# Optimization experiments

Hardware: AMD Instinct MI355X
Metric: run time of the kernel (lower is better)

## Reference

```python
import jax, jax.numpy as jnp
import numpy as np

N_NODES = 50000
N_EDGES = 800000
MUL = 16            # multiplicity of each irrep (16x0e + 16x1o)
RADIAL_IN = 8       # radial basis size
RADIAL_HID = 64
N_PATHS = 5         # TP paths: s*Y0->s, v.Yv->s, s*Yv->v, v*Y0->v, v x Yv->v
NUM_SPECIES = 4
AVG_NEIGH = 16.0


def setup_inputs() -> dict:
    key = jax.random.key(0)
    ks = jax.random.split(key, 16)
    inp = {
        'node_scalars': jax.random.normal(ks[0], (N_NODES, MUL), jnp.float32),
        'node_vectors': jax.random.normal(ks[1], (N_NODES, MUL * 3), jnp.float32),
        'edge_sh': jax.random.normal(ks[2], (N_EDGES, 4), jnp.float32),
        'radial_emb': jax.random.uniform(ks[3], (N_EDGES, RADIAL_IN), jnp.float32),
        'senders': jax.random.randint(ks[4], (N_EDGES,), 0, N_NODES, jnp.int32),
        'receivers': jax.random.randint(ks[5], (N_EDGES,), 0, N_NODES, jnp.int32),
        'species': jax.random.randint(ks[6], (N_NODES,), 0, NUM_SPECIES, jnp.int32),
        # learned params (fan-in scaled)
        'W_in_s': jax.random.normal(ks[7], (MUL, MUL), jnp.float32) / np.sqrt(MUL),
        'W_in_v': jax.random.normal(ks[8], (MUL, MUL), jnp.float32) / np.sqrt(MUL),
        'mlp_w1': jax.random.normal(ks[9], (RADIAL_IN, RADIAL_HID), jnp.float32) / np.sqrt(RADIAL_IN),
        'mlp_b1': jnp.zeros((RADIAL_HID,), jnp.float32),
        'mlp_w2': jax.random.normal(ks[10], (RADIAL_HID, N_PATHS * MUL), jnp.float32) / np.sqrt(RADIAL_HID),
        'W_out_s': jax.random.normal(ks[11], (2 * MUL, 2 * MUL), jnp.float32) / np.sqrt(2 * MUL),
        'W_out_v': jax.random.normal(ks[12], (3 * MUL, MUL), jnp.float32) / np.sqrt(3 * MUL),
        'sc_s': jax.random.normal(ks[13], (NUM_SPECIES, MUL, 2 * MUL), jnp.float32) / np.sqrt(MUL),
        'sc_v': jax.random.normal(ks[14], (NUM_SPECIES, MUL, MUL), jnp.float32) / np.sqrt(MUL),
    }
    return inp


def reference(node_scalars, node_vectors, edge_sh, radial_emb, senders, receivers,
              species, W_in_s, W_in_v, mlp_w1, mlp_b1, mlp_w2, W_out_s, W_out_v,
              sc_s, sc_v):
    N = node_scalars.shape[0]
    inv_sqrt_deg = 1.0 / np.sqrt(AVG_NEIGH)

    # ---- input per-irrep linear ----
    s = node_scalars @ W_in_s                                  # [N,16]
    v_in = node_vectors.reshape(N, MUL, 3)
    v = jnp.einsum('nuc,uw->nwc', v_in, W_in_v)                # [N,16,3]

    # ---- gather sender features ----
    xs = s[senders]                                            # [E,16]
    xv = v[senders]                                            # [E,16,3]
    Y0 = edge_sh[:, :1]                                        # [E,1] l=0 SH
    Yv = edge_sh[:, 1:4]                                       # [E,3] l=1 SH

    # ---- radial MLP -> per-path tensor-product weights ----
    h = jax.nn.silu(radial_emb @ mlp_w1 + mlp_b1)              # [E,64]
    w = (h @ mlp_w2).reshape(-1, N_PATHS, MUL)                 # [E,5,16]

    # ---- CG tensor product (uvu) messages ----
    m_s1 = w[:, 0] * xs * Y0                                   # 0e x 0e -> 0e
    m_s2 = w[:, 1] * jnp.einsum('euc,ec->eu', xv, Yv)          # 1o x 1o -> 0e (dot)
    m_v1 = w[:, 2, :, None] * xs[:, :, None] * Yv[:, None, :]  # 0e x 1o -> 1o
    m_v2 = w[:, 3, :, None] * xv * Y0[:, :, None]              # 1o x 0e -> 1o
    m_v3 = w[:, 4, :, None] * jnp.cross(xv, Yv[:, None, :])    # 1o x 1o -> 1o (cross)

    # ---- scatter-sum to receivers + neighbour normalization ----
    m_s = jnp.concatenate([m_s1, m_s2], axis=-1)               # [E,32]
    m_v = jnp.concatenate([m_v1, m_v2, m_v3], axis=1)          # [E,48,3]
    a_s = jax.ops.segment_sum(m_s, receivers, num_segments=N) * inv_sqrt_deg
    a_v = jax.ops.segment_sum(m_v, receivers, num_segments=N) * inv_sqrt_deg

    # ---- output per-irrep linear ----
    pre_s = a_s @ W_out_s                                      # [N,32]
    pre_v = jnp.einsum('nuc,uw->nwc', a_v, W_out_v)            # [N,16,3]

    # ---- species-dependent self connection ----
    pre_s = pre_s + jnp.einsum('nu,nuw->nw', node_scalars, sc_s[species])
    pre_v = pre_v + jnp.einsum('nuc,nuw->nwc', v_in, sc_v[species])

    # ---- gate nonlinearity ----
    out_s = jax.nn.silu(pre_s[:, :MUL])                        # scalar outputs
    gates = jax.nn.sigmoid(pre_s[:, MUL:])                     # gate scalars
    out_v = pre_v * gates[:, :, None]

    # ---- resnet ----
    out_s = out_s + node_scalars
    out_v = out_v + v_in

    return jnp.concatenate([out_s, out_v.reshape(N, MUL * 3)], axis=-1)
```

## Files before the change

kernel.cpp:

```cpp
#include <hip/hip_runtime.h>
#include <hip/hip_bf16.h>

typedef unsigned short u16;
typedef unsigned int   u32;
typedef _Float16 h2 __attribute__((ext_vector_type(2)));
typedef short s8v __attribute__((ext_vector_type(8)));
typedef float f4v __attribute__((ext_vector_type(4)));
typedef u16 u16x4 __attribute__((ext_vector_type(4)));

#define N_NODES 50000
#define N_EDGES 800000
#define NCH   4
#define RPC   12500
#define CHMAX 204800

#define RPB   250
#define NBINS 200
#define EPB   4096
#define NBB   ((N_EDGES+EPB-1)/EPB)

#define WB_W1H  0
#define WB_B1   256
#define WB_W2F  320
#define WB_WINS 2880
#define WB_WINV 3136
#define WB_WOS  3392
#define WB_WOV  4416
#define WB_SCS  5184
#define WB_SCV  7232
#define WB_FLAG 8256
#define OFF_SV16 8260
#define IDX_BCNT 1608260
#define IDX_BOF2 1608516
#define IDX_BCUR 1608772
#define IDX_OFFS 1658260
#define IDX_BUCK 1758262
#define OFF_WP   2558264
#define ACC_OFF  15665472
#define IDX_EEID 17865472
#define OFF_ER16 18665472

__device__ __forceinline__ float bf2f(u16 v){
  union { u32 u; float f; } x; x.u = ((u32)v) << 16; return x.f;
}
__device__ __forceinline__ u16 f2bf(float f){
  u32 u = __float_as_uint(f);
  u32 lsb = (u >> 16) & 1u;
  u32 r = u + 0x7fffu + lsb;
  return (u16)(r >> 16);
}
__device__ __forceinline__ float ldx(const void* p, long long i, int isf){
  return isf ? ((const float*)p)[i] : bf2f(((const u16*)p)[i]);
}
__device__ __forceinline__ u32 pkh2(float a, float b){
  union { u32 u; h2 v; } x; x.v.x = (_Float16)a; x.v.y = (_Float16)b; return x.u;
}
__device__ __forceinline__ float dot2(h2 a, u32 w, float c){
  union { u32 u; h2 v; } x; x.u = w;
#if __has_builtin(__builtin_amdgcn_fdot2)
  return __builtin_amdgcn_fdot2(a, x.v, c, false);
#else
  return c + (float)a.x*(float)x.v.x + (float)a.y*(float)x.v.y;
#endif
}
__device__ __forceinline__ float sigmoidf_(float x){ return 1.f/(1.f + __expf(-x)); }

__global__ void detect_dtype(const u32* __restrict__ remb_raw, int* __restrict__ flag){
  int t = threadIdx.x;
  u32 w = remb_raw[t];
  u32 lo = w & 0xffffu, hi = w >> 16;
  int okl = ((lo & 0x8000u) == 0) && (((lo >> 7) & 0xffu) <= 126u);
  int okh = ((hi & 0x8000u) == 0) && (((hi >> 7) & 0xffu) <= 126u);
  unsigned long long bad = __ballot(!(okl && okh));
  if (t == 0) *flag = (bad != 0ull) ? 1 : 0;
}

__global__ void prep_weights(const void* __restrict__ w1, const void* __restrict__ b1g,
                             const void* __restrict__ w2, const void* __restrict__ wins,
                             const void* __restrict__ winv, const void* __restrict__ wos,
                             const void* __restrict__ wov, const void* __restrict__ scs,
                             const void* __restrict__ scv, float* __restrict__ wbuf,
                             const int* __restrict__ flag){
  int t = threadIdx.x;
  int isf = *flag;
  u32* w1h  = (u32*)(wbuf + WB_W1H);
  u16* w2f  = (u16*)(wbuf + WB_W2F);
  for (int idx=t; idx<256;  idx+=256){
    int j = idx>>2, ip = idx&3;
    w1h[idx] = pkh2(ldx(w1, (2*ip)*64+j, isf), ldx(w1, (2*ip+1)*64+j, isf));
  }
  for (int idx=t; idx<64;   idx+=256){ wbuf[WB_B1+idx]  = ldx(b1g, idx, isf); }
  for (int idx=t; idx<5120; idx+=256){
    int tt = idx >> 10;
    int rem = idx & 1023;
    int kh = rem >> 9;
    int rem2 = rem & 511;
    int ln = rem2 >> 3, j = rem2 & 7;
    int k = kh*32 + (ln>>4)*8 + j;
    int o = tt*16 + (ln&15);
    w2f[idx] = f2bf(ldx(w2, (long long)k*80 + o, isf));
  }
  for (int idx=t; idx<256;  idx+=256){ wbuf[WB_WINS+idx] = ldx(wins, idx, isf); }
  for (int idx=t; idx<256;  idx+=256){ wbuf[WB_WINV+idx] = ldx(winv, idx, isf); }
  for (int idx=t; idx<1024; idx+=256){ wbuf[WB_WOS+idx]  = ldx(wos, idx, isf); }
  for (int idx=t; idx<768;  idx+=256){ wbuf[WB_WOV+idx]  = ldx(wov, idx, isf); }
  for (int idx=t; idx<2048; idx+=256){ wbuf[WB_SCS+idx]  = ldx(scs, idx, isf); }
  for (int idx=t; idx<1024; idx+=256){ wbuf[WB_SCV+idx]  = ldx(scv, idx, isf); }
}

__global__ void __launch_bounds__(64) node_pre(
    const void* __restrict__ ns_g, const void* __restrict__ nv_g,
    const float* __restrict__ wbuf, u16* __restrict__ sv16,
    const int* __restrict__ flag){
  int n = blockIdx.x*64 + threadIdx.x;
  if (n >= N_NODES) return;
  int isf = *flag;
  float a[16], b[48];
  if (isf){
    const f4v* pa = (const f4v*)ns_g + (size_t)n*4;
    #pragma unroll
    for (int k=0;k<4;k++){
      f4v v = pa[k];
      a[k*4]=v[0]; a[k*4+1]=v[1]; a[k*4+2]=v[2]; a[k*4+3]=v[3];
    }
    const f4v* pb = (const f4v*)nv_g + (size_t)n*12;
    #pragma unroll
    for (int k=0;k<12;k++){
      f4v v = pb[k];
      b[k*4]=v[0]; b[k*4+1]=v[1]; b[k*4+2]=v[2]; b[k*4+3]=v[3];
    }
  } else {
    const s8v* pa = (const s8v*)ns_g + (size_t)n*2;
    #pragma unroll
    for (int k=0;k<2;k++){
      s8v v = pa[k];
      #pragma unroll
      for (int j=0;j<8;j++) a[k*8+j] = bf2f((u16)v[j]);
    }
    const s8v* pb = (const s8v*)nv_g + (size_t)n*6;
    #pragma unroll
    for (int k=0;k<6;k++){
      s8v v = pb[k];
      #pragma unroll
      for (int j=0;j<8;j++) b[k*8+j] = bf2f((u16)v[j]);
    }
  }
  const float* wins = wbuf + WB_WINS;
  const float* winv = wbuf + WB_WINV;
  float s[16];
  #pragma unroll
  for (int w=0;w<16;w++) s[w]=0.f;
  #pragma unroll
  for (int u=0;u<16;u++){
    float au = a[u];
    #pragma unroll
    for (int w=0;w<16;w++) s[w] += au * wins[u*16+w];
  }
  float v0[16], v1[16], v2[16];
  #pragma unroll
  for (int w=0;w<16;w++){ v0[w]=0.f; v1[w]=0.f; v2[w]=0.f; }
  #pragma unroll
  for (int u=0;u<16;u++){
    float bu0=b[u*3], bu1=b[u*3+1], bu2=b[u*3+2];
    #pragma unroll
    for (int w=0;w<16;w++){
      float wv = winv[u*16+w];
      v0[w] += bu0*wv; v1[w] += bu1*wv; v2[w] += bu2*wv;
    }
  }
  s8v* svp = (s8v*)(sv16 + (size_t)n*64);
  #pragma unroll
  for (int w=0;w<16;w+=2){
    s8v pk;
    pk[0]=(short)f2bf(s[w]);   pk[1]=(short)f2bf(v0[w]);
    pk[2]=(short)f2bf(v1[w]);  pk[3]=(short)f2bf(v2[w]);
    pk[4]=(short)f2bf(s[w+1]); pk[5]=(short)f2bf(v0[w+1]);
    pk[6]=(short)f2bf(v1[w+1]);pk[7]=(short)f2bf(v2[w+1]);
    svp[w>>1] = pk;
  }
}

__global__ void __launch_bounds__(256) bin_count(const int* __restrict__ receivers,
                                                 int* __restrict__ bcnt){
  __shared__ int lcnt[NBINS];
  int t = threadIdx.x;
  for (int i=t;i<NBINS;i+=256) lcnt[i]=0;
  __syncthreads();
  int base = blockIdx.x*EPB;
  for (int i=t;i<EPB;i+=256){
    int e = base+i;
    if (e<N_EDGES) atomicAdd(&lcnt[receivers[e]/RPB],1);
  }
  __syncthreads();
  for (int i=t;i<NBINS;i+=256) if (lcnt[i]) atomicAdd(&bcnt[i], lcnt[i]);
}

__global__ void bin_scan(const int* __restrict__ bcnt, int* __restrict__ binoff,
                         int* __restrict__ bincur, int* __restrict__ offs){
  __shared__ int lds[NBINS];
  int t=threadIdx.x;
  if (t<NBINS) lds[t]=bcnt[t];
  __syncthreads();
  for (int off=1; off<NBINS; off<<=1){
    int v = (t<NBINS && t>=off)? lds[t-off] : 0;
    __syncthreads();
    if (t<NBINS) lds[t]+=v;
    __syncthreads();
  }
  if (t<NBINS){ int ex = lds[t]-bcnt[t]; binoff[t]=ex; bincur[t]=ex; }
  if (t==0) offs[N_NODES] = N_EDGES;
}

__global__ void __launch_bounds__(256) bin_scatter(const int* __restrict__ receivers,
                 int* __restrict__ bincur, u32* __restrict__ eeid, u16* __restrict__ er){
  __shared__ int lcnt[NBINS], loff[NBINS], lcur[NBINS], gbase[NBINS];
  __shared__ u32 seid[EPB];
  __shared__ u16 sr[EPB];
  int t = threadIdx.x;
  for (int i=t;i<NBINS;i+=256) lcnt[i]=0;
  __syncthreads();
  int base = blockIdx.x*EPB;
  int r_[16];
  #pragma unroll
  for (int k=0;k<16;k++){
    int e = base + t + k*256;
    r_[k] = (e<N_EDGES)? receivers[e] : -1;
    if (r_[k]>=0) atomicAdd(&lcnt[r_[k]/RPB],1);
  }
  __syncthreads();
  if (t<NBINS) loff[t]=lcnt[t];
  __syncthreads();
  for (int off=1; off<NBINS; off<<=1){
    int v=(t<NBINS&&t>=off)?loff[t-off]:0;
    __syncthreads();
    if (t<NBINS) loff[t]+=v;
    __syncthreads();
  }
  if (t<NBINS){
    int ex=loff[t]-lcnt[t]; loff[t]=ex; lcur[t]=ex;
    gbase[t] = lcnt[t] ? atomicAdd(&bincur[t], lcnt[t]) : 0;
  }
  __syncthreads();
  #pragma unroll
  for (int k=0;k<16;k++){
    if (r_[k]>=0){
      int b=r_[k]/RPB;
      int p=atomicAdd(&lcur[b],1);
      seid[p]=(u32)(base + t + k*256);
      sr[p]=(u16)r_[k];
    }
  }
  __syncthreads();
  int rem = N_EDGES - base;
  int tot = rem < EPB ? rem : EPB;
  for (int i=t;i<tot;i+=256){
    int b = sr[i]/RPB;
    int dst = gbase[b] + (i - loff[b]);
    eeid[dst]=seid[i]; er[dst]=sr[i];
  }
}

__global__ void __launch_bounds__(256) bin_finalize(const u32* __restrict__ eeid,
        const u16* __restrict__ er, const int* __restrict__ binoff,
        const int* __restrict__ bcnt, int* __restrict__ offs, int* __restrict__ bucket){
  __shared__ int deg[RPB], pfx[RPB], lcur[RPB];
  int b=blockIdx.x, t=threadIdx.x;
  int beg=binoff[b], cnt=bcnt[b];
  for (int i=t;i<RPB;i+=256) deg[i]=0;
  __syncthreads();
  int r0=b*RPB;
  for (int i=t;i<cnt;i+=256) atomicAdd(&deg[er[beg+i]-r0],1);
  __syncthreads();
  if (t<RPB) pfx[t]=deg[t];
  __syncthreads();
  for (int off=1; off<RPB; off<<=1){
    int v=(t<RPB&&t>=off)?pfx[t-off]:0;
    __syncthreads();
    if (t<RPB) pfx[t]+=v;
    __syncthreads();
  }
  if (t<RPB){
    int ex=pfx[t]-deg[t]; pfx[t]=ex; lcur[t]=ex;
    offs[r0+t]=beg+ex;
  }
  __syncthreads();
  for (int i=t;i<cnt;i+=256){
    int rr = er[beg+i]-r0;
    int k = atomicAdd(&lcur[rr],1);
    bucket[beg+k] = (int)eeid[beg+i];
  }
}

__global__ void __launch_bounds__(256) pass1_w(
    const int* __restrict__ bucket, const int* __restrict__ offs,
    const void* __restrict__ remb, const float* __restrict__ wbuf,
    u16* __restrict__ wp16, int rlo, const int* __restrict__ flag){
  __shared__ u16 hlds[4*16*72];
  int tid = threadIdx.x;
  int lane = tid & 63, wid = tid >> 6;
  int isf = *flag;
  int chunkBeg = offs[rlo], chunkEnd = offs[rlo + RPC];
  int r0e = chunkBeg + (blockIdx.x*4 + wid)*16;
  if (r0e >= chunkEnd) return;
  u16* hw = hlds + wid*(16*72);
  int e = lane & 15, q = lane >> 4;

  int er = r0e + e;
  int eid = (er < chunkEnd) ? bucket[er] : 0;
  float re[8];
  if (isf){
    f4v ra = ((const f4v*)remb)[(size_t)eid*2];
    f4v rb = ((const f4v*)remb)[(size_t)eid*2+1];
    re[0]=ra[0]; re[1]=ra[1]; re[2]=ra[2]; re[3]=ra[3];
    re[4]=rb[0]; re[5]=rb[1]; re[6]=rb[2]; re[7]=rb[3];
  } else {
    s8v r8 = ((const s8v*)remb)[eid];
    #pragma unroll
    for (int i=0;i<8;i++) re[i] = bf2f((u16)r8[i]);
  }
  h2 reh[4];
  #pragma unroll
  for (int ip=0;ip<4;ip++){ reh[ip].x=(_Float16)re[2*ip]; reh[ip].y=(_Float16)re[2*ip+1]; }
  const u32* w1h = (const u32*)(wbuf + WB_W1H);
  const float* b1 = wbuf + WB_B1;
  #pragma unroll
  for (int jj=0;jj<16;jj++){
    int j = q*16 + jj;
    float a = b1[j];
    #pragma unroll
    for (int ip=0;ip<4;ip++) a = dot2(reh[ip], w1h[j*4+ip], a);
    a = a * sigmoidf_(a);
    hw[e*72 + j] = f2bf(a);
  }
  asm volatile("s_waitcnt lgkmcnt(0)" ::: "memory");

  const u16* w2f = (const u16*)(wbuf + WB_W2F);
  s8v bfr[5][2];
  #pragma unroll
  for (int t=0;t<5;t++)
    #pragma unroll
    for (int kh=0;kh<2;kh++)
      bfr[t][kh] = *(const s8v*)(w2f + ((t*2+kh)*64 + lane)*8);

  f4v acc[5];
  #pragma unroll
  for (int t=0;t<5;t++) acc[t] = (f4v){0.f,0.f,0.f,0.f};
  #pragma unroll
  for (int kh=0;kh<2;kh++){
    s8v af = *(const s8v*)(hw + e*72 + kh*32 + q*8);
    #pragma unroll
    for (int t=0;t<5;t++)
      acc[t] = __builtin_amdgcn_mfma_f32_16x16x32_bf16(af, bfr[t][kh], acc[t], 0,0,0);
  }
  int n = lane & 15;
  #pragma unroll
  for (int r=0;r<4;r++){
    int er2 = r0e + q*4 + r;
    if (er2 < chunkEnd){
      size_t widx = (size_t)(er2 - chunkBeg);
      s8v pk;
      pk[0]=(short)f2bf(acc[0][r]); pk[1]=(short)f2bf(acc[1][r]);
      pk[2]=(short)f2bf(acc[2][r]); pk[3]=(short)f2bf(acc[3][r]);
      pk[4]=(short)f2bf(acc[4][r]); pk[5]=0; pk[6]=0; pk[7]=0;
      *(s8v*)(wp16 + (widx*16 + n)*8) = pk;
    }
  }
}

__global__ void __launch_bounds__(256, 4) pass2_reduce(
    const int* __restrict__ bucket, const int* __restrict__ offs,
    const void* __restrict__ edge_sh, const int* __restrict__ senders,
    const u16* __restrict__ sv16, const u16* __restrict__ wp16,
    float* __restrict__ accbuf, int rlo, const int* __restrict__ flag){
  int tid = threadIdx.x;
  int lane = tid & 63, wid = tid >> 6;
  int u = lane & 15, q = lane >> 4;
  int isf = *flag;
  int r = rlo + blockIdx.x*4 + wid;
  int chunkBeg = offs[rlo];
  int beg = offs[r], end = offs[r+1];
  float As0=0.f,As1=0.f;
  float Av00=0.f,Av01=0.f,Av02=0.f, Av10=0.f,Av11=0.f,Av12=0.f, Av20=0.f,Av21=0.f,Av22=0.f;
  auto body = [&](int rank){
    int eid = bucket[rank];
    float Y0,Yv0,Yv1,Yv2;
    if (isf){
      f4v y = ((const f4v*)edge_sh)[eid];
      Y0=y[0]; Yv0=y[1]; Yv1=y[2]; Yv2=y[3];
    } else {
      u16x4 y = ((const u16x4*)edge_sh)[eid];
      Y0=bf2f(y[0]); Yv0=bf2f(y[1]); Yv1=bf2f(y[2]); Yv2=bf2f(y[3]);
    }
    int snd = senders[eid];
    s8v wv = *(const s8v*)(wp16 + ((size_t)(rank - chunkBeg)*16 + u)*8);
    float w0=bf2f((u16)wv[0]), w1=bf2f((u16)wv[1]), w2=bf2f((u16)wv[2]);
    float w3=bf2f((u16)wv[3]), w4=bf2f((u16)wv[4]);
    u16x4 sv = *(const u16x4*)(sv16 + ((size_t)snd*16 + u)*4);
    float xs=bf2f(sv[0]), x0=bf2f(sv[1]), x1=bf2f(sv[2]), x2=bf2f(sv[3]);
    As0 += w0*xs*Y0;
    As1 += w1*(x0*Yv0 + x1*Yv1 + x2*Yv2);
    float t1 = w2*xs;  Av00 += t1*Yv0; Av01 += t1*Yv1; Av02 += t1*Yv2;
    float t2 = w3*Y0;  Av10 += t2*x0;  Av11 += t2*x1;  Av12 += t2*x2;
    Av20 += w4*(x1*Yv2 - x2*Yv1);
    Av21 += w4*(x2*Yv0 - x0*Yv2);
    Av22 += w4*(x0*Yv1 - x1*Yv0);
  };
  int rank = beg + q;
  for (; rank + 4 < end; rank += 8){ body(rank); body(rank+4); }
  if (rank < end) body(rank);
  #define RED2(x) { x += __shfl_xor(x,16); x += __shfl_xor(x,32); }
  RED2(As0) RED2(As1)
  RED2(Av00) RED2(Av01) RED2(Av02)
  RED2(Av10) RED2(Av11) RED2(Av12)
  RED2(Av20) RED2(Av21) RED2(Av22)
  #undef RED2
  float* ab = accbuf + (size_t)(r - rlo)*176;
  if (q == 0){ ab[u]=As0;    ab[32+u]=Av00;  ab[112+u]=Av21; }
  else if (q == 1){ ab[16+u]=As1; ab[80+u]=Av01;  ab[144+u]=Av12; }
  else if (q == 2){ ab[48+u]=Av10; ab[128+u]=Av02; ab[160+u]=Av22; }
  else            { ab[64+u]=Av20; ab[96+u]=Av11; }
}

__global__ void __launch_bounds__(256) pass2_epilogue(
    const float* __restrict__ accbuf, const float* __restrict__ wbuf,
    const void* __restrict__ ns_g, const void* __restrict__ nv_g,
    const int* __restrict__ species, void* __restrict__ out,
    int rlo, const int* __restrict__ flag){
  __shared__ float sb[16*176 + 16*16 + 16*48];
  int tid = threadIdx.x;
  int isf = *flag;
  int n0 = rlo + blockIdx.x*16;
  int rem = rlo + RPC - n0;
  int nblk = rem < 16 ? rem : 16;
  {
    int tot = nblk*176;
    const float* src = accbuf + (size_t)(n0 - rlo)*176;
    for (int i=tid; i<tot; i+=256) sb[i] = src[i];
    float* nsb = sb + 2816;
    for (int i=tid; i<nblk*16; i+=256)
      nsb[i] = ldx(ns_g, (long long)n0*16 + i, isf);
    float* vinb = sb + 2816 + 256;
    for (int i=tid; i<nblk*48; i+=256)
      vinb[i] = ldx(nv_g, (long long)n0*48 + i, isf);
  }
  __syncthreads();
  int g = tid >> 4, u = tid & 15;
  if (g >= nblk) return;
  int nn = n0 + g;
  const float* bin  = sb + g*176;
  const float* nsb  = sb + 2816 + g*16;
  const float* vinb = sb + 2816 + 256 + g*48;
  int sp = species[nn];
  const float* wos = wbuf + WB_WOS;
  const float* scs = wbuf + WB_SCS + sp*512;
  const float* wov = wbuf + WB_WOV;
  const float* scv = wbuf + WB_SCV + sp*256;
  float p0 = 0.f, p1 = 0.f;
  #pragma unroll
  for (int j=0;j<32;j++){
    float a = bin[j]*0.25f;
    p0 += a*wos[j*32+u];
    p1 += a*wos[j*32+16+u];
  }
  #pragma unroll
  for (int j=0;j<16;j++){
    float nu = nsb[j];
    p0 += nu*scs[j*32+u];
    p1 += nu*scs[j*32+16+u];
  }
  float gate = sigmoidf_(p1);
  float os = p0*sigmoidf_(p0) + nsb[u];
  float pv0, pv1, pv2;
  {
    float a0=0.f, a1=0.f, a2=0.f;
    #pragma unroll
    for (int j=0;j<48;j++){
      float wv = wov[j*16+u];
      a0 += bin[32 + 0*48 + j]*0.25f*wv;
      a1 += bin[32 + 1*48 + j]*0.25f*wv;
      a2 += bin[32 + 2*48 + j]*0.25f*wv;
    }
    #pragma unroll
    for (int j=0;j<16;j++){
      float sv = scv[j*16+u];
      a0 += vinb[j*3+0]*sv;
      a1 += vinb[j*3+1]*sv;
      a2 += vinb[j*3+2]*sv;
    }
    pv0 = a0*gate + vinb[u*3+0];
    pv1 = a1*gate + vinb[u*3+1];
    pv2 = a2*gate + vinb[u*3+2];
  }
  if (isf){
    float* orow = (float*)out + (size_t)nn*64;
    orow[u] = os;
    orow[16 + u*3 + 0] = pv0;
    orow[16 + u*3 + 1] = pv1;
    orow[16 + u*3 + 2] = pv2;
  } else {
    u16* orow = (u16*)out + (size_t)nn*64;
    orow[u] = f2bf(os);
    orow[16 + u*3 + 0] = f2bf(pv0);
    orow[16 + u*3 + 1] = f2bf(pv1);
    orow[16 + u*3 + 2] = f2bf(pv2);
  }
}

extern "C" void kernel_launch(void* const* d_in, const int* in_sizes, int n_in,
                              void* d_out, int out_size, void* d_ws, size_t ws_size,
                              hipStream_t stream){
  const void* node_scalars = d_in[0];
  const void* node_vectors = d_in[1];
  const void* edge_sh      = d_in[2];
  const void* radial_emb   = d_in[3];
  const int* senders      = (const int*)d_in[4];
  const int* receivers    = (const int*)d_in[5];
  const int* species      = (const int*)d_in[6];
  const void* W_in_s  = d_in[7];
  const void* W_in_v  = d_in[8];
  const void* mlp_w1  = d_in[9];
  const void* mlp_b1  = d_in[10];
  const void* mlp_w2  = d_in[11];
  const void* W_out_s = d_in[12];
  const void* W_out_v = d_in[13];
  const void* sc_s    = d_in[14];
  const void* sc_v    = d_in[15];

  float* wsf  = (float*)d_ws;
  int*   wsi  = (int*)d_ws;
  u32*   wsu  = (u32*)d_ws;
  float* wbuf = wsf;
  u16*   sv16 = (u16*)(wsu + OFF_SV16);
  int*   bcnt = wsi + IDX_BCNT;
  int*   bof2 = wsi + IDX_BOF2;
  int*   bcur = wsi + IDX_BCUR;
  int*   offs = wsi + IDX_OFFS;
  int*   buck = wsi + IDX_BUCK;
  u16*   wp16 = (u16*)(wsu + OFF_WP);
  float* accb = wsf + ACC_OFF;
  u32*   eeid = wsu + IDX_EEID;
  u16*   er16 = (u16*)(wsu + OFF_ER16);
  int*   flag = (int*)(wbuf + WB_FLAG);

  detect_dtype<<<1,64,0,stream>>>((const u32*)radial_emb, flag);
  hipMemsetAsync(bcnt, 0, NBINS*sizeof(int), stream);
  prep_weights<<<1,256,0,stream>>>(mlp_w1, mlp_b1, mlp_w2, W_in_s, W_in_v,
                                   W_out_s, W_out_v, sc_s, sc_v, wbuf, flag);
  node_pre<<<(N_NODES+63)/64,64,0,stream>>>(node_scalars, node_vectors, wbuf,
                                            sv16, flag);
  bin_count<<<NBB,256,0,stream>>>(receivers, bcnt);
  bin_scan<<<1,256,0,stream>>>(bcnt, bof2, bcur, offs);
  bin_scatter<<<NBB,256,0,stream>>>(receivers, bcur, eeid, er16);
  bin_finalize<<<NBINS,256,0,stream>>>(eeid, er16, bof2, bcnt, offs, buck);
  for (int c = 0; c < NCH; c++){
    int rlo = c * RPC;
    pass1_w<<<CHMAX/64, 256, 0, stream>>>(buck, offs, radial_emb, wbuf, wp16, rlo, flag);
    pass2_reduce<<<RPC/4, 256, 0, stream>>>(buck, offs, edge_sh, senders,
                                            sv16, wp16, accb, rlo, flag);
    pass2_epilogue<<<(RPC+15)/16, 256, 0, stream>>>(accb, wbuf, node_scalars,
                                                    node_vectors, species,
                                                    d_out, rlo, flag);
  }
}
```

Measured before the change: 435.4 us.

## Fuse radial MLP, message reduction and epilogue into one per-node-block kernel

```diff
diff --git a/kernel.cpp b/kernel.cpp
--- a/kernel.cpp
+++ b/kernel.cpp
@@ -10,9 +10,6 @@
 
 #define N_NODES 50000
 #define N_EDGES 800000
-#define NCH   4
-#define RPC   12500
-#define CHMAX 204800
 
 #define RPB   250
 #define NBINS 200
@@ -35,10 +32,8 @@
 #define IDX_BCUR 1608772
 #define IDX_OFFS 1658260
 #define IDX_BUCK 1758262
-#define OFF_WP   2558264
-#define ACC_OFF  15665472
-#define IDX_EEID 17865472
-#define OFF_ER16 18665472
+#define IDX_EEID 2558264
+#define OFF_ER16 3358264
 
 __device__ __forceinline__ float bf2f(u16 v){
   union { u32 u; float f; } x; x.u = ((u32)v) << 16; return x.f;
@@ -291,49 +286,38 @@
   }
 }
 
-__global__ void __launch_bounds__(256) pass1_w(
+__global__ void __launch_bounds__(256) fused_edge(
     const int* __restrict__ bucket, const int* __restrict__ offs,
-    const void* __restrict__ remb, const float* __restrict__ wbuf,
-    u16* __restrict__ wp16, int rlo, const int* __restrict__ flag){
+    const void* __restrict__ remb, const void* __restrict__ edge_sh,
+    const int* __restrict__ senders, const u16* __restrict__ sv16,
+    const float* __restrict__ wbuf, const void* __restrict__ ns_g,
+    const void* __restrict__ nv_g, const int* __restrict__ species,
+    void* __restrict__ out, const int* __restrict__ flag){
   __shared__ u16 hlds[4*16*72];
+  __shared__ float bins[16*176];
+  __shared__ int offs_l[17];
+  __shared__ float sb2[16*16 + 16*48];
   int tid = threadIdx.x;
   int lane = tid & 63, wid = tid >> 6;
   int isf = *flag;
-  int chunkBeg = offs[rlo], chunkEnd = offs[rlo + RPC];
-  int r0e = chunkBeg + (blockIdx.x*4 + wid)*16;
-  if (r0e >= chunkEnd) return;
+  int n0 = blockIdx.x * 16;
+  if (tid < 17) offs_l[tid] = offs[n0 + tid];
+  for (int i=tid; i<16*176; i+=256) bins[i] = 0.f;
+  __syncthreads();
+  {
+    float* nsb = sb2;
+    for (int i=tid; i<256; i+=256)
+      nsb[i] = ldx(ns_g, (long long)n0*16 + i, isf);
+    float* vinb = sb2 + 256;
+    for (int i=tid; i<768; i+=256)
+      vinb[i] = ldx(nv_g, (long long)n0*48 + i, isf);
+  }
+  int beg = offs_l[0], end = offs_l[16];
+  int cnt = end - beg;
   u16* hw = hlds + wid*(16*72);
   int e = lane & 15, q = lane >> 4;
-
-  int er = r0e + e;
-  int eid = (er < chunkEnd) ? bucket[er] : 0;
-  float re[8];
-  if (isf){
-    f4v ra = ((const f4v*)remb)[(size_t)eid*2];
-    f4v rb = ((const f4v*)remb)[(size_t)eid*2+1];
-    re[0]=ra[0]; re[1]=ra[1]; re[2]=ra[2]; re[3]=ra[3];
-    re[4]=rb[0]; re[5]=rb[1]; re[6]=rb[2]; re[7]=rb[3];
-  } else {
-    s8v r8 = ((const s8v*)remb)[eid];
-    #pragma unroll
-    for (int i=0;i<8;i++) re[i] = bf2f((u16)r8[i]);
-  }
-  h2 reh[4];
-  #pragma unroll
-  for (int ip=0;ip<4;ip++){ reh[ip].x=(_Float16)re[2*ip]; reh[ip].y=(_Float16)re[2*ip+1]; }
   const u32* w1h = (const u32*)(wbuf + WB_W1H);
   const float* b1 = wbuf + WB_B1;
-  #pragma unroll
-  for (int jj=0;jj<16;jj++){
-    int j = q*16 + jj;
-    float a = b1[j];
-    #pragma unroll
-    for (int ip=0;ip<4;ip++) a = dot2(reh[ip], w1h[j*4+ip], a);
-    a = a * sigmoidf_(a);
-    hw[e*72 + j] = f2bf(a);
-  }
-  asm volatile("s_waitcnt lgkmcnt(0)" ::: "memory");
-
   const u16* w2f = (const u16*)(wbuf + WB_W2F);
   s8v bfr[5][2];
   #pragma unroll
@@ -342,114 +326,90 @@
     for (int kh=0;kh<2;kh++)
       bfr[t][kh] = *(const s8v*)(w2f + ((t*2+kh)*64 + lane)*8);
 
-  f4v acc[5];
-  #pragma unroll
-  for (int t=0;t<5;t++) acc[t] = (f4v){0.f,0.f,0.f,0.f};
-  #pragma unroll
-  for (int kh=0;kh<2;kh++){
-    s8v af = *(const s8v*)(hw + e*72 + kh*32 + q*8);
-    #pragma unroll
-    for (int t=0;t<5;t++)
-      acc[t] = __builtin_amdgcn_mfma_f32_16x16x32_bf16(af, bfr[t][kh], acc[t], 0,0,0);
-  }
-  int n = lane & 15;
-  #pragma unroll
-  for (int r=0;r<4;r++){
-    int er2 = r0e + q*4 + r;
-    if (er2 < chunkEnd){
-      size_t widx = (size_t)(er2 - chunkBeg);
-      s8v pk;
-      pk[0]=(short)f2bf(acc[0][r]); pk[1]=(short)f2bf(acc[1][r]);
-      pk[2]=(short)f2bf(acc[2][r]); pk[3]=(short)f2bf(acc[3][r]);
-      pk[4]=(short)f2bf(acc[4][r]); pk[5]=0; pk[6]=0; pk[7]=0;
-      *(s8v*)(wp16 + (widx*16 + n)*8) = pk;
-    }
-  }
-}
-
-__global__ void __launch_bounds__(256, 4) pass2_reduce(
-    const int* __restrict__ bucket, const int* __restrict__ offs,
-    const void* __restrict__ edge_sh, const int* __restrict__ senders,
-    const u16* __restrict__ sv16, const u16* __restrict__ wp16,
-    float* __restrict__ accbuf, int rlo, const int* __restrict__ flag){
-  int tid = threadIdx.x;
-  int lane = tid & 63, wid = tid >> 6;
-  int u = lane & 15, q = lane >> 4;
-  int isf = *flag;
-  int r = rlo + blockIdx.x*4 + wid;
-  int chunkBeg = offs[rlo];
-  int beg = offs[r], end = offs[r+1];
-  float As0=0.f,As1=0.f;
-  float Av00=0.f,Av01=0.f,Av02=0.f, Av10=0.f,Av11=0.f,Av12=0.f, Av20=0.f,Av21=0.f,Av22=0.f;
-  auto body = [&](int rank){
-    int eid = bucket[rank];
-    float Y0,Yv0,Yv1,Yv2;
+  for (int tb = wid*16; tb < cnt; tb += 64){
+    int er = beg + tb + e;
+    int eid = (er < end) ? bucket[er] : 0;
+    float re[8];
     if (isf){
-      f4v y = ((const f4v*)edge_sh)[eid];
-      Y0=y[0]; Yv0=y[1]; Yv1=y[2]; Yv2=y[3];
+      f4v ra = ((const f4v*)remb)[(size_t)eid*2];
+      f4v rb = ((const f4v*)remb)[(size_t)eid*2+1];
+      re[0]=ra[0]; re[1]=ra[1]; re[2]=ra[2]; re[3]=ra[3];
+      re[4]=rb[0]; re[5]=rb[1]; re[6]=rb[2]; re[7]=rb[3];
     } else {
-      u16x4 y = ((const u16x4*)edge_sh)[eid];
-      Y0=bf2f(y[0]); Yv0=bf2f(y[1]); Yv1=bf2f(y[2]); Yv2=bf2f(y[3]);
-    }
-    int snd = senders[eid];
-    s8v wv = *(const s8v*)(wp16 + ((size_t)(rank - chunkBeg)*16 + u)*8);
-    float w0=bf2f((u16)wv[0]), w1=bf2f((u16)wv[1]), w2=bf2f((u16)wv[2]);
-    float w3=bf2f((u16)wv[3]), w4=bf2f((u16)wv[4]);
-    u16x4 sv = *(const u16x4*)(sv16 + ((size_t)snd*16 + u)*4);
-    float xs=bf2f(sv[0]), x0=bf2f(sv[1]), x1=bf2f(sv[2]), x2=bf2f(sv[3]);
-    As0 += w0*xs*Y0;
-    As1 += w1*(x0*Yv0 + x1*Yv1 + x2*Yv2);
-    float t1 = w2*xs;  Av00 += t1*Yv0; Av01 += t1*Yv1; Av02 += t1*Yv2;
-    float t2 = w3*Y0;  Av10 += t2*x0;  Av11 += t2*x1;  Av12 += t2*x2;
-    Av20 += w4*(x1*Yv2 - x2*Yv1);
-    Av21 += w4*(x2*Yv0 - x0*Yv2);
-    Av22 += w4*(x0*Yv1 - x1*Yv0);
-  };
-  int rank = beg + q;
-  for (; rank + 4 < end; rank += 8){ body(rank); body(rank+4); }
-  if (rank < end) body(rank);
-  #define RED2(x) { x += __shfl_xor(x,16); x += __shfl_xor(x,32); }
-  RED2(As0) RED2(As1)
-  RED2(Av00) RED2(Av01) RED2(Av02)
-  RED2(Av10) RED2(Av11) RED2(Av12)
-  RED2(Av20) RED2(Av21) RED2(Av22)
-  #undef RED2
-  float* ab = accbuf + (size_t)(r - rlo)*176;
-  if (q == 0){ ab[u]=As0;    ab[32+u]=Av00;  ab[112+u]=Av21; }
-  else if (q == 1){ ab[16+u]=As1; ab[80+u]=Av01;  ab[144+u]=Av12; }
-  else if (q == 2){ ab[48+u]=Av10; ab[128+u]=Av02; ab[160+u]=Av22; }
-  else            { ab[64+u]=Av20; ab[96+u]=Av11; }
-}
-
-__global__ void __launch_bounds__(256) pass2_epilogue(
-    const float* __restrict__ accbuf, const float* __restrict__ wbuf,
-    const void* __restrict__ ns_g, const void* __restrict__ nv_g,
-    const int* __restrict__ species, void* __restrict__ out,
-    int rlo, const int* __restrict__ flag){
-  __shared__ float sb[16*176 + 16*16 + 16*48];
-  int tid = threadIdx.x;
-  int isf = *flag;
-  int n0 = rlo + blockIdx.x*16;
-  int rem = rlo + RPC - n0;
-  int nblk = rem < 16 ? rem : 16;
-  {
-    int tot = nblk*176;
-    const float* src = accbuf + (size_t)(n0 - rlo)*176;
-    for (int i=tid; i<tot; i+=256) sb[i] = src[i];
-    float* nsb = sb + 2816;
-    for (int i=tid; i<nblk*16; i+=256)
-      nsb[i] = ldx(ns_g, (long long)n0*16 + i, isf);
-    float* vinb = sb + 2816 + 256;
-    for (int i=tid; i<nblk*48; i+=256)
-      vinb[i] = ldx(nv_g, (long long)n0*48 + i, isf);
-  }
-  __syncthreads();
-  int g = tid >> 4, u = tid & 15;
-  if (g >= nblk) return;
-  int nn = n0 + g;
-  const float* bin  = sb + g*176;
-  const float* nsb  = sb + 2816 + g*16;
-  const float* vinb = sb + 2816 + 256 + g*48;
+      s8v r8 = ((const s8v*)remb)[eid];
+      #pragma unroll
+      for (int i=0;i<8;i++) re[i] = bf2f((u16)r8[i]);
+    }
+    h2 reh[4];
+    #pragma unroll
+    for (int ip=0;ip<4;ip++){ reh[ip].x=(_Float16)re[2*ip]; reh[ip].y=(_Float16)re[2*ip+1]; }
+    asm volatile("s_waitcnt lgkmcnt(0)" ::: "memory");
+    #pragma unroll
+    for (int jj=0;jj<16;jj++){
+      int j = q*16 + jj;
+      float a = b1[j];
+      #pragma unroll
+      for (int ip=0;ip<4;ip++) a = dot2(reh[ip], w1h[j*4+ip], a);
+      a = a * sigmoidf_(a);
+      hw[e*72 + j] = f2bf(a);
+    }
+    asm volatile("s_waitcnt lgkmcnt(0)" ::: "memory");
+    f4v acc[5];
+    #pragma unroll
+    for (int t=0;t<5;t++) acc[t] = (f4v){0.f,0.f,0.f,0.f};
+    #pragma unroll
+    for (int kh=0;kh<2;kh++){
+      s8v af = *(const s8v*)(hw + e*72 + kh*32 + q*8);
+      #pragma unroll
+      for (int t=0;t<5;t++)
+        acc[t] = __builtin_amdgcn_mfma_f32_16x16x32_bf16(af, bfr[t][kh], acc[t], 0,0,0);
+    }
+    int u = e;
+    #pragma unroll
+    for (int r=0;r<4;r++){
+      int rank2 = beg + tb + q*4 + r;
+      if (rank2 < end){
+        int eidr = __shfl(eid, q*4 + r);
+        float Y0,Yv0,Yv1,Yv2;
+        if (isf){
+          f4v y = ((const f4v*)edge_sh)[eidr];
+          Y0=y[0]; Yv0=y[1]; Yv1=y[2]; Yv2=y[3];
+        } else {
+          u16x4 y = ((const u16x4*)edge_sh)[eidr];
+          Y0=bf2f(y[0]); Yv0=bf2f(y[1]); Yv1=bf2f(y[2]); Yv2=bf2f(y[3]);
+        }
+        int snd = senders[eidr];
+        u16x4 sv = *(const u16x4*)(sv16 + ((size_t)snd*16 + u)*4);
+        float xs=bf2f(sv[0]), x0=bf2f(sv[1]), x1=bf2f(sv[2]), x2=bf2f(sv[3]);
+        float w0=acc[0][r], w1=acc[1][r], w2=acc[2][r], w3=acc[3][r], w4=acc[4][r];
+        int g = 0;
+        if (rank2 >= offs_l[g+8]) g += 8;
+        if (rank2 >= offs_l[g+4]) g += 4;
+        if (rank2 >= offs_l[g+2]) g += 2;
+        if (rank2 >= offs_l[g+1]) g += 1;
+        float* bp = bins + g*176;
+        float t1 = w2*xs, t2 = w3*Y0;
+        atomicAdd(&bp[u],      w0*xs*Y0);
+        atomicAdd(&bp[16+u],   w1*(x0*Yv0 + x1*Yv1 + x2*Yv2));
+        atomicAdd(&bp[32+u],   t1*Yv0);
+        atomicAdd(&bp[80+u],   t1*Yv1);
+        atomicAdd(&bp[128+u],  t1*Yv2);
+        atomicAdd(&bp[48+u],   t2*x0);
+        atomicAdd(&bp[96+u],   t2*x1);
+        atomicAdd(&bp[144+u],  t2*x2);
+        atomicAdd(&bp[64+u],   w4*(x1*Yv2 - x2*Yv1));
+        atomicAdd(&bp[112+u],  w4*(x2*Yv0 - x0*Yv2));
+        atomicAdd(&bp[160+u],  w4*(x0*Yv1 - x1*Yv0));
+      }
+    }
+  }
+  __syncthreads();
+
+  int g2 = tid >> 4, u2 = tid & 15;
+  int nn = n0 + g2;
+  const float* bin  = bins + g2*176;
+  const float* nsb  = sb2 + g2*16;
+  const float* vinb = sb2 + 256 + g2*48;
   int sp = species[nn];
   const float* wos = wbuf + WB_WOS;
   const float* scs = wbuf + WB_SCS + sp*512;
@@ -459,50 +419,50 @@
   #pragma unroll
   for (int j=0;j<32;j++){
     float a = bin[j]*0.25f;
-    p0 += a*wos[j*32+u];
-    p1 += a*wos[j*32+16+u];
+    p0 += a*wos[j*32+u2];
+    p1 += a*wos[j*32+16+u2];
   }
   #pragma unroll
   for (int j=0;j<16;j++){
     float nu = nsb[j];
-    p0 += nu*scs[j*32+u];
-    p1 += nu*scs[j*32+16+u];
+    p0 += nu*scs[j*32+u2];
+    p1 += nu*scs[j*32+16+u2];
   }
   float gate = sigmoidf_(p1);
-  float os = p0*sigmoidf_(p0) + nsb[u];
+  float os = p0*sigmoidf_(p0) + nsb[u2];
   float pv0, pv1, pv2;
   {
     float a0=0.f, a1=0.f, a2=0.f;
     #pragma unroll
     for (int j=0;j<48;j++){
-      float wv = wov[j*16+u];
+      float wv = wov[j*16+u2];
       a0 += bin[32 + 0*48 + j]*0.25f*wv;
       a1 += bin[32 + 1*48 + j]*0.25f*wv;
       a2 += bin[32 + 2*48 + j]*0.25f*wv;
     }
     #pragma unroll
     for (int j=0;j<16;j++){
-      float sv = scv[j*16+u];
+      float sv = scv[j*16+u2];
       a0 += vinb[j*3+0]*sv;
       a1 += vinb[j*3+1]*sv;
       a2 += vinb[j*3+2]*sv;
     }
-    pv0 = a0*gate + vinb[u*3+0];
-    pv1 = a1*gate + vinb[u*3+1];
-    pv2 = a2*gate + vinb[u*3+2];
+    pv0 = a0*gate + vinb[u2*3+0];
+    pv1 = a1*gate + vinb[u2*3+1];
+    pv2 = a2*gate + vinb[u2*3+2];
   }
   if (isf){
     float* orow = (float*)out + (size_t)nn*64;
-    orow[u] = os;
-    orow[16 + u*3 + 0] = pv0;
-    orow[16 + u*3 + 1] = pv1;
-    orow[16 + u*3 + 2] = pv2;
+    orow[u2] = os;
+    orow[16 + u2*3 + 0] = pv0;
+    orow[16 + u2*3 + 1] = pv1;
+    orow[16 + u2*3 + 2] = pv2;
   } else {
     u16* orow = (u16*)out + (size_t)nn*64;
-    orow[u] = f2bf(os);
-    orow[16 + u*3 + 0] = f2bf(pv0);
-    orow[16 + u*3 + 1] = f2bf(pv1);
-    orow[16 + u*3 + 2] = f2bf(pv2);
+    orow[u2] = f2bf(os);
+    orow[16 + u2*3 + 0] = f2bf(pv0);
+    orow[16 + u2*3 + 1] = f2bf(pv1);
+    orow[16 + u2*3 + 2] = f2bf(pv2);
   }
 }
 
@@ -536,8 +496,6 @@
   int*   bcur = wsi + IDX_BCUR;
   int*   offs = wsi + IDX_OFFS;
   int*   buck = wsi + IDX_BUCK;
-  u16*   wp16 = (u16*)(wsu + OFF_WP);
-  float* accb = wsf + ACC_OFF;
   u32*   eeid = wsu + IDX_EEID;
   u16*   er16 = (u16*)(wsu + OFF_ER16);
   int*   flag = (int*)(wbuf + WB_FLAG);
@@ -552,13 +510,8 @@
   bin_scan<<<1,256,0,stream>>>(bcnt, bof2, bcur, offs);
   bin_scatter<<<NBB,256,0,stream>>>(receivers, bcur, eeid, er16);
   bin_finalize<<<NBINS,256,0,stream>>>(eeid, er16, bof2, bcnt, offs, buck);
-  for (int c = 0; c < NCH; c++){
-    int rlo = c * RPC;
-    pass1_w<<<CHMAX/64, 256, 0, stream>>>(buck, offs, radial_emb, wbuf, wp16, rlo, flag);
-    pass2_reduce<<<RPC/4, 256, 0, stream>>>(buck, offs, edge_sh, senders,
-                                            sv16, wp16, accb, rlo, flag);
-    pass2_epilogue<<<(RPC+15)/16, 256, 0, stream>>>(accb, wbuf, node_scalars,
-                                                    node_vectors, species,
-                                                    d_out, rlo, flag);
-  }
-}
+  fused_edge<<<N_NODES/16, 256, 0, stream>>>(buck, offs, radial_emb, edge_sh,
+                                             senders, sv16, wbuf,
+                                             node_scalars, node_vectors, species,
+                                             d_out, flag);
+}
```

Measured after the change: 982.5 us. 2.26x slower.
